# Kernel optimization log

Hardware: AMD Instinct MI355X
Metric: run time of the kernel (lower is better)

## Reference

```python
import jax, jax.numpy as jnp
import numpy as np

B, C, N, K = 8, 3, 4096, 20
EPS = 1e-5

def bn(x, g, b, axes):
    # training-mode batch norm: normalize over batch/spatial axes, channel last
    m = jnp.mean(x, axes, keepdims=True)
    v = jnp.var(x, axes, keepdims=True)
    return g * (x - m) * jax.lax.rsqrt(v + EPS) + b

def setup_inputs() -> dict:
    key = jax.random.key(0)
    ks = jax.random.split(key, 8)
    def xav(kk, shape):
        fan_out, fan_in = shape
        lim = (6.0 / (fan_in + fan_out)) ** 0.5
        return jax.random.uniform(kk, shape, minval=-lim, maxval=lim, dtype=jnp.float32)
    return dict(
        x=jax.random.normal(ks[0], (B, C, N), dtype=jnp.float32),
        w1=xav(ks[1], (64, 2 * C)), g1=jnp.ones(64), b1=jnp.zeros(64),
        w2=xav(ks[2], (128, 64)), g2=jnp.ones(128), b2=jnp.zeros(128),
        w3=xav(ks[3], (1024, 128)), g3=jnp.ones(1024), b3=jnp.zeros(1024),
        w4=xav(ks[4], (512, 1024)), g4=jnp.ones(512), b4=jnp.zeros(512),
        w5=xav(ks[5], (256, 512)), g5=jnp.ones(256), b5=jnp.zeros(256),
        wl=jnp.zeros((9, 256), dtype=jnp.float32),  # zero-init per reset_parameters
        bl=jnp.zeros(9, dtype=jnp.float32),
    )

def reference(x, w1, g1, b1, w2, g2, b2, w3, g3, b3, w4, g4, b4, w5, g5, b5, wl, bl):
    xt = jnp.transpose(x, (0, 2, 1))  # (B, N, C)
    sq = jnp.sum(xt * xt, -1)  # (B, N)
    # negative squared pairwise distance: -(|a|^2 - 2ab + |b|^2)
    nd = 2.0 * jnp.einsum('bnc,bmc->bnm', xt, xt) - sq[:, :, None] - sq[:, None, :]
    _, idx = jax.lax.top_k(nd, K)  # (B, N, K) nearest neighbors (includes self)
    nbr = jax.vmap(lambda pts, ids: pts[ids])(xt, idx)  # (B, N, K, C)
    ctr = xt[:, :, None, :]
    edge = jnp.concatenate([jnp.broadcast_to(ctr, (B, N, K, C)), nbr - ctr], -1)  # (B,N,K,2C)
    # EdgeConv shared MLP (1x1 conv + BN + ReLU), then max over k
    h = jax.nn.relu(bn(jnp.einsum('bnkc,oc->bnko', edge, w1), g1, b1, (0, 1, 2)))
    h = jax.nn.relu(bn(jnp.einsum('bnkc,oc->bnko', h, w2), g2, b2, (0, 1, 2)))
    h = jnp.max(h, 2)  # (B, N, 128)
    # local shared MLP then global max pool over points
    h = jax.nn.relu(bn(jnp.einsum('bnc,oc->bno', h, w3), g3, b3, (0, 1)))
    h = jnp.max(h, 1)  # (B, 1024)
    # global MLP
    h = jax.nn.relu(bn(h @ w4.T, g4, b4, (0,)))
    h = jax.nn.relu(bn(h @ w5.T, g5, b5, (0,)))
    y = (h @ wl.T + bl).reshape(B, 3, 3)
    return y + jnp.eye(3, dtype=y.dtype)
```

## Files before the change

### kernel.cpp

```cpp
#include <hip/hip_runtime.h>

#define NPTS 4096
#define KNN 20
#define CNT1f 655360.0f
#define CNT3f 32768.0f
#define BNEPS 1e-5f

#define OFF_IDX   0
#define OFF_M     655360
#define OFF_ES    655360
#define OFF_G1P   656384
#define OFF_S1P   672768
#define ZERO1_BEG 655360
#define ZERO1_CNT 17664
#define OFF_W2B   2752512
#define OFF_W3B   2756608
#define OFF_XP    2822144
#define OFF_G3P   2953216
#define OFF_SM3P  2985984
#define OFF_GMAX  2986240
#define OFF_Z4    2994432
#define ZG3_BEG   2953216
#define ZG3_CNT   41216
#define OFF_SC1   4849664
#define OFF_SH1   4849728
#define OFF_SC2   4849792
#define OFF_SH2   4849920
#define OFF_SC3   4850048
#define OFF_SH3   4851072
#define OFF_Z5    4856192
#define OFF_W1B   4858240

typedef float f32x4 __attribute__((ext_vector_type(4)));
typedef short s16x8 __attribute__((ext_vector_type(8)));

__device__ __forceinline__ unsigned short f2bf(float f) {
    unsigned u = __float_as_uint(f);
    return (unsigned short)((u + 0x7FFFu + ((u >> 16) & 1u)) >> 16);
}

__global__ __launch_bounds__(256) void k_initprep(const float* __restrict__ x,
                                                  const float* __restrict__ w1,
                                                  const float* __restrict__ w2,
                                                  const float* __restrict__ w3, float* W) {
    int i = blockIdx.x * 256 + threadIdx.x;
    unsigned short* w1b = (unsigned short*)(W + OFF_W1B);
    unsigned short* w2b = (unsigned short*)(W + OFF_W2B);
    unsigned short* w3b = (unsigned short*)(W + OFF_W3B);
    w3b[i] = f2bf(w3[i]);
    if (i < 8192) w2b[i] = f2bf(w2[i]);
    if (i < 2048) {
        int c = i >> 5, k = i & 31;
        w1b[i] = (k < 6) ? f2bf(w1[c * 6 + k]) : (unsigned short)0;
    }
    if (i < ZERO1_CNT) W[ZERO1_BEG + i] = 0.0f;
    if (i < ZG3_CNT) W[ZG3_BEG + i] = 0.0f;
    if (i < 32768) {
        int b = i >> 12, j = i & 4095;
        float4 p;
        p.x = x[b * 12288 + j];
        p.y = x[b * 12288 + 4096 + j];
        p.z = x[b * 12288 + 8192 + j];
        p.w = 0.f;
        ((float4*)(W + OFF_XP))[i] = p;
    }
}

template <int PER>
__device__ __forceinline__ void wave_scan_find(const int* H, int K, int lane,
                                               int& B, int& below, int& hB) {
    int c[PER]; int s = 0;
    const int base = lane * PER;
#pragma unroll
    for (int p = 0; p < PER; ++p) { c[p] = H[base + p]; s += c[p]; }
    int pre = s;
#pragma unroll
    for (int off = 1; off < 64; off <<= 1) {
        int t = __shfl_up(pre, off, 64);
        if (lane >= off) pre += t;
    }
    int excl = pre - s;
    bool has = (excl < K) && (K <= excl + s);
    unsigned long long m = __ballot(has);
    int src = (int)(__ffsll((unsigned long long)m) - 1);
    int mb = 0, mbelow = 0, mh = 0;
    if (lane == src) {
        int cum = excl;
#pragma unroll
        for (int p = 0; p < PER; ++p) {
            if (cum < K && K <= cum + c[p]) { mb = base + p; mbelow = cum; mh = c[p]; break; }
            cum += c[p];
        }
    }
    B = __shfl(mb, src, 64);
    below = __shfl(mbelow, src, 64);
    hB = __shfl(mh, src, 64);
}

__global__ __launch_bounds__(256) void k_knn(int* __restrict__ idx, float* W) {
    __shared__ int hist[4][1024];
    __shared__ int outi[4][20];
    __shared__ int cnts[4][2];
    __shared__ float estat[27];
    const int tid = threadIdx.x;
    const int b = blockIdx.y;
    const float4* xb4 = ((const float4*)(W + OFF_XP)) + b * NPTS;
    if (tid < 27) estat[tid] = 0.f;
    if (tid < 8) cnts[tid >> 1][tid & 1] = 0;
    const int wv = tid >> 6, lane = tid & 63;
    const int q = blockIdx.x * 4 + wv;
    const float4 qp = xb4[q];
    int* H = hist[wv];
    unsigned int key[64];
    unsigned int mymin = 0xFFFFFFFFu;
#pragma unroll
    for (int p = 0; p < 16; ++p) H[lane * 16 + p] = 0;
#pragma unroll
    for (int it = 0; it < 64; ++it) {
        int j = it * 64 + lane;
        float4 pp = xb4[j];
        float dx = pp.x - qp.x, dy = pp.y - qp.y, dz = pp.z - qp.z;
        float d = fmaf(dx, dx, fmaf(dy, dy, dz * dz));
        unsigned int u = (j == q) ? 0xFFFFFFFFu : __float_as_uint(d);
        key[it] = u;
        mymin = mymin < u ? mymin : u;
    }
    __syncthreads();
#pragma unroll
    for (int off = 32; off; off >>= 1) {
        unsigned int o = (unsigned int)__shfl_xor((int)mymin, off);
        mymin = mymin < o ? mymin : o;
    }
    const unsigned int base = mymin;
#pragma unroll
    for (int it = 0; it < 64; ++it) {
        unsigned int t9 = key[it] - base;
        unsigned int bin = t9 >> 19; if (bin > 1023u) bin = 1023u;
        atomicAdd(&H[bin], 1);
    }
    int B, below, hB;
    wave_scan_find<16>(H, KNN - 1, lane, B, below, hB);
    unsigned int P = (unsigned int)B;
    int rem = (KNN - 1) - below;
    int S = 19;
    if (hB != rem) {
#pragma unroll
        for (int p = 0; p < 8; ++p) H[lane * 8 + p] = 0;
#pragma unroll
        for (int it = 0; it < 64; ++it) {
            unsigned int t9 = key[it] - base;
            unsigned int b0 = t9 >> 19; if (b0 > 1023u) b0 = 1023u;
            if (b0 == P) atomicAdd(&H[(t9 >> 10) & 511], 1);
        }
        wave_scan_find<8>(H, rem, lane, B, below, hB);
        P = (P << 9) | (unsigned int)B;
        rem -= below;
        S = 10;
        if (hB != rem) {
#pragma unroll
            for (int p = 0; p < 8; ++p) H[lane * 8 + p] = 0;
#pragma unroll
            for (int it = 0; it < 64; ++it) {
                unsigned int t9 = key[it] - base;
                if ((t9 >> 10) == P) atomicAdd(&H[(t9 >> 1) & 511], 1);
            }
            wave_scan_find<8>(H, rem, lane, B, below, hB);
            P = (P << 9) | (unsigned int)B;
            rem -= below;
            S = 1;
        }
    }
    int* OC = cnts[wv];
#pragma unroll
    for (int it = 0; it < 64; ++it) {
        unsigned int t9 = key[it] - base;
        unsigned int v;
        if (S == 19) { v = t9 >> 19; if (v > 1023u) v = 1023u; }
        else v = t9 >> S;
        if (v <= P) {
            bool take = v < P;
            if (!take) { int e = atomicAdd(&OC[1], 1); take = (e < rem); }
            if (take) { int pos = atomicAdd(&OC[0], 1); outi[wv][pos] = it * 64 + lane; }
        }
    }
    if (lane == 0) outi[wv][KNN - 1] = q;
    const int obase = (b * NPTS + q) * KNN;
    if (lane < KNN) idx[obase + lane] = outi[wv][lane];
    float st[27];
#pragma unroll
    for (int v = 0; v < 27; ++v) st[v] = 0.f;
    if (lane < KNN) {
        int j = outi[wv][lane];
        float4 np = xb4[j];
        float e[6];
        e[0] = qp.x; e[1] = qp.y; e[2] = qp.z;
        e[3] = np.x - qp.x; e[4] = np.y - qp.y; e[5] = np.z - qp.z;
        int id = 6;
#pragma unroll
        for (int i = 0; i < 6; ++i) {
            st[i] = e[i];
#pragma unroll
            for (int jj = i; jj < 6; ++jj) { st[id] = e[i] * e[jj]; id++; }
        }
    }
#pragma unroll
    for (int v = 0; v < 27; ++v) {
        float s = st[v];
        s += __shfl_xor(s, 32); s += __shfl_xor(s, 16); s += __shfl_xor(s, 8);
        s += __shfl_xor(s, 4);  s += __shfl_xor(s, 2);  s += __shfl_xor(s, 1);
        st[v] = s;
    }
    if (lane == 0) {
#pragma unroll
        for (int v = 0; v < 27; ++v) atomicAdd(&estat[v], st[v]);
    }
    __syncthreads();
    if (tid < 27) atomicAdd(&W[OFF_ES + (blockIdx.x & 31) * 32 + tid], estat[tid]);
}

__global__ __launch_bounds__(256) void k_gram1(const int* __restrict__ idx,
                                               const float* __restrict__ w1,
                                               const float* __restrict__ g1,
                                               const float* __restrict__ b1, float* W) {
    __shared__ unsigned short h1t[80 * 136];
    __shared__ unsigned short eda[128 * 32];
    __shared__ float sc1s[64], sh1s[64];
    __shared__ float es[27];
    const int t = threadIdx.x;
    const int b = blockIdx.x >> 6;
    const int ebase_b = (blockIdx.x & 63) * 1280;
    const float4* xpb = ((const float4*)(W + OFF_XP)) + b * NPTS;
    const unsigned short* w1b = (const unsigned short*)(W + OFF_W1B);
    if (t < 27) {
        float s = 0.f;
        for (int p = 0; p < 32; ++p) s += W[OFF_ES + p * 32 + t];
        es[t] = s;
    }
    __syncthreads();
    if (t < 64) {
        float wr[6];
#pragma unroll
        for (int i = 0; i < 6; ++i) wr[i] = w1[t * 6 + i];
        float m = 0.f;
#pragma unroll
        for (int i = 0; i < 6; ++i) m += wr[i] * es[i];
        m *= (1.f / CNT1f);
        float qv = 0.f;
        int id = 6;
#pragma unroll
        for (int i = 0; i < 6; ++i)
#pragma unroll
            for (int jj = 0; jj < 6; ++jj)
                if (jj >= i) { qv += (jj == i ? 1.f : 2.f) * wr[i] * wr[jj] * es[id]; id++; }
        qv *= (1.f / CNT1f);
        float var = qv - m * m;
        float sc = g1[t] * rsqrtf(var + BNEPS);
        sc1s[t] = sc;
        sh1s[t] = b1[t] - m * sc;
        if (blockIdx.x == 0) { W[OFF_SC1 + t] = sc; W[OFF_SH1 + t] = sh1s[t]; }
    }
    for (int i = t; i < 2048; i += 256) {
        int rr = i >> 7, e = i & 127;
        h1t[(64 + rr) * 136 + e] = (rr == 0) ? (unsigned short)0x3F80 : (unsigned short)0;
    }
    const int w = t >> 6, lane = t & 63, n16 = lane & 15, quad = lane >> 4;
    s16x8 Bw1[4];
#pragma unroll
    for (int nt = 0; nt < 4; ++nt)
        Bw1[nt] = *(const s16x8*)&w1b[(nt * 16 + n16) * 32 + quad * 8];
    f32x4 acc[5];
#pragma unroll
    for (int j = 0; j < 5; ++j) acc[j] = (f32x4){0.f, 0.f, 0.f, 0.f};
    for (int ck = 0; ck < 10; ++ck) {
        __syncthreads();
        if (t < 128) {
            int e_l = ebase_b + ck * 128 + t;
            int q = e_l / KNN;
            int jn = idx[b * (NPTS * KNN) + e_l];
            float4 c = xpb[q];
            float4 n = xpb[jn];
            float E[6];
            E[0] = c.x; E[1] = c.y; E[2] = c.z;
            E[3] = n.x - c.x; E[4] = n.y - c.y; E[5] = n.z - c.z;
            unsigned short* row = &eda[t * 32];
#pragma unroll
            for (int k = 0; k < 6; ++k) row[k] = f2bf(E[k]);
#pragma unroll
            for (int k = 6; k < 32; ++k) row[k] = 0;
        }
        __syncthreads();
#pragma unroll
        for (int i2 = 0; i2 < 2; ++i2) {
            int tt = w + 4 * i2;
            s16x8 Af = *(const s16x8*)&eda[(tt * 16 + n16) * 32 + quad * 8];
#pragma unroll
            for (int nt = 0; nt < 4; ++nt) {
                f32x4 z = (f32x4){0.f, 0.f, 0.f, 0.f};
                z = __builtin_amdgcn_mfma_f32_16x16x32_bf16(Af, Bw1[nt], z, 0, 0, 0);
                int chan = nt * 16 + n16;
                float sc = sc1s[chan], sh = sh1s[chan];
#pragma unroll
                for (int r = 0; r < 4; ++r) {
                    float h = sc * z[r] + sh;
                    h1t[chan * 136 + tt * 16 + quad * 4 + r] = f2bf(h > 0.f ? h : 0.f);
                }
            }
        }
        __syncthreads();
#pragma unroll
        for (int ks = 0; ks < 4; ++ks) {
            s16x8 Af = *(const s16x8*)&h1t[(w * 16 + n16) * 136 + ks * 32 + quad * 8];
#pragma unroll
            for (int jt = 0; jt < 5; ++jt) {
                s16x8 Bf = *(const s16x8*)&h1t[(jt * 16 + n16) * 136 + ks * 32 + quad * 8];
                acc[jt] = __builtin_amdgcn_mfma_f32_16x16x32_bf16(Af, Bf, acc[jt], 0, 0, 0);
            }
        }
    }
    const int part = blockIdx.x & 3;
    const int gi = w * 16 + quad * 4;
#pragma unroll
    for (int jt = 0; jt < 4; ++jt)
#pragma unroll
        for (int r = 0; r < 4; ++r)
            atomicAdd(&W[OFF_G1P + part * 4096 + (gi + r) * 64 + jt * 16 + n16], acc[jt][r]);
    if (n16 == 0) {
#pragma unroll
        for (int r = 0; r < 4; ++r)
            atomicAdd(&W[OFF_S1P + part * 64 + gi + r], acc[4][r]);
    }
}

__global__ __launch_bounds__(256) void k_fin2(const float* __restrict__ w2, const float* __restrict__ g2,
                                              const float* __restrict__ b2, float* W) {
    __shared__ float Gs[4096];
    __shared__ float s1s[64];
    __shared__ float w2s[128 * 65];
    const int t = threadIdx.x;
    for (int i = t; i < 4096; i += 256)
        Gs[i] = W[OFF_G1P + i] + W[OFF_G1P + 4096 + i] + W[OFF_G1P + 8192 + i] + W[OFF_G1P + 12288 + i];
    if (t < 64) s1s[t] = W[OFF_S1P + t] + W[OFF_S1P + 64 + t] + W[OFF_S1P + 128 + t] + W[OFF_S1P + 192 + t];
    for (int i = t; i < 8192; i += 256) w2s[(i >> 6) * 65 + (i & 63)] = w2[i];
    __syncthreads();
    const int c = t >> 1, half = t & 1;
    float acc = 0.f;
    for (int ii = 0; ii < 32; ++ii) {
        int i = 32 * half + ii;
        float wi = w2s[c * 65 + i];
        float inner = 0.f;
        for (int j = 0; j < 64; ++j) inner += Gs[i * 64 + j] * w2s[c * 65 + j];
        acc += wi * inner;
    }
    acc += __shfl_xor(acc, 1);
    if (half == 0) {
        float ms = 0.f;
        for (int j = 0; j < 64; ++j) ms += w2s[c * 65 + j] * s1s[j];
        float mean = ms * (1.f / CNT1f);
        float var = acc * (1.f / CNT1f) - mean * mean;
        float sc = g2[c] * rsqrtf(var + BNEPS);
        W[OFF_SC2 + c] = sc;
        W[OFF_SH2 + c] = b2[c] - mean * sc;
    }
}

__global__ __launch_bounds__(256) void k_c2apply(const int* __restrict__ idx, float* W) {
    __shared__ unsigned short h1b[256 * 72];
    __shared__ unsigned short eda[160 * 32];
    __shared__ float sc1s[64], sh1s[64];
    const int t = threadIdx.x;
    const int b = blockIdx.y, q0 = blockIdx.x * 8;
    const float4* xpb = ((const float4*)(W + OFF_XP)) + b * NPTS;
    const int ebase = (b * NPTS + q0) * KNN;
    const unsigned short* w2b = (const unsigned short*)(W + OFF_W2B);
    const unsigned short* w1b = (const unsigned short*)(W + OFF_W1B);
    if (t < 64) { sc1s[t] = W[OFF_SC1 + t]; sh1s[t] = W[OFF_SH1 + t]; }
    if (t < 160) {
        int q = q0 + t / KNN;
        int jn = idx[ebase + t];
        float4 c = xpb[q];
        float4 n = xpb[jn];
        float E[6];
        E[0] = c.x; E[1] = c.y; E[2] = c.z;
        E[3] = n.x - c.x; E[4] = n.y - c.y; E[5] = n.z - c.z;
        unsigned short* row = &eda[t * 32];
#pragma unroll
        for (int k = 0; k < 6; ++k) row[k] = f2bf(E[k]);
#pragma unroll
        for (int k = 6; k < 32; ++k) row[k] = 0;
    }
    const int w = t >> 6, lane = t & 63, n16 = lane & 15, quad = lane >> 4;
    s16x8 Bw1[4];
#pragma unroll
    for (int nt = 0; nt < 4; ++nt)
        Bw1[nt] = *(const s16x8*)&w1b[(nt * 16 + n16) * 32 + quad * 8];
    __syncthreads();
#pragma unroll
    for (int i2 = 0; i2 < 4; ++i2) {
        int tt = w + 4 * i2;
        int row = tt * 16 + n16;
        int q = row >> 5, kk = row & 31;
        s16x8 Af = (s16x8){0, 0, 0, 0, 0, 0, 0, 0};
        if (kk < 20) Af = *(const s16x8*)&eda[(q * 20 + kk) * 32 + quad * 8];
#pragma unroll
        for (int nt = 0; nt < 4; ++nt) {
            f32x4 z = (f32x4){0.f, 0.f, 0.f, 0.f};
            z = __builtin_amdgcn_mfma_f32_16x16x32_bf16(Af, Bw1[nt], z, 0, 0, 0);
            int chan = nt * 16 + n16;
            float sc = sc1s[chan], sh = sh1s[chan];
#pragma unroll
            for (int r = 0; r < 4; ++r) {
                float h = sc * z[r] + sh;
                h1b[(tt * 16 + quad * 4 + r) * 72 + chan] = f2bf(h > 0.f ? h : 0.f);
            }
        }
    }
    __syncthreads();
    unsigned short* Mb = (unsigned short*)(W + OFF_M);
#pragma unroll
    for (int nt_i = 0; nt_i < 2; ++nt_i) {
        const int nt = 2 * w + nt_i;
        const int chan = nt * 16 + n16;
        const float sc2 = W[OFF_SC2 + chan], sh2 = W[OFF_SH2 + chan];
        s16x8 Bf0 = *(const s16x8*)&w2b[chan * 64 + quad * 8];
        s16x8 Bf1 = *(const s16x8*)&w2b[chan * 64 + 32 + quad * 8];
#pragma unroll
        for (int q = 0; q < 8; ++q) {
            f32x4 accA = (f32x4){0.f, 0.f, 0.f, 0.f};
            f32x4 accB = (f32x4){0.f, 0.f, 0.f, 0.f};
            s16x8 a0 = *(const s16x8*)&h1b[(q * 32 + n16) * 72 + quad * 8];
            s16x8 a1 = *(const s16x8*)&h1b[(q * 32 + 16 + n16) * 72 + quad * 8];
            accA = __builtin_amdgcn_mfma_f32_16x16x32_bf16(a0, Bf0, accA, 0, 0, 0);
            accB = __builtin_amdgcn_mfma_f32_16x16x32_bf16(a1, Bf0, accB, 0, 0, 0);
            a0 = *(const s16x8*)&h1b[(q * 32 + n16) * 72 + 32 + quad * 8];
            a1 = *(const s16x8*)&h1b[(q * 32 + 16 + n16) * 72 + 32 + quad * 8];
            accA = __builtin_amdgcn_mfma_f32_16x16x32_bf16(a0, Bf1, accA, 0, 0, 0);
            accB = __builtin_amdgcn_mfma_f32_16x16x32_bf16(a1, Bf1, accB, 0, 0, 0);
            float mx = 0.f;
#pragma unroll
            for (int r = 0; r < 4; ++r) {
                float h = sc2 * accA[r] + sh2;
                mx = fmaxf(mx, h > 0.f ? h : 0.f);
            }
            if (quad == 0) {
#pragma unroll
                for (int r = 0; r < 4; ++r) {
                    float h = sc2 * accB[r] + sh2;
                    mx = fmaxf(mx, h > 0.f ? h : 0.f);
                }
            }
            mx = fmaxf(mx, __shfl_xor(mx, 16));
            mx = fmaxf(mx, __shfl_xor(mx, 32));
            if (quad == 0)
                Mb[(b * NPTS + q0 + q) * 128 + chan] = f2bf(mx);
        }
    }
}

__global__ __launch_bounds__(256) void k_gram3(float* W) {
    __shared__ unsigned short Mt[128 * 72];
    const int t = threadIdx.x;
    const int w = t >> 6, lane = t & 63, n16 = lane & 15, quad = lane >> 4;
    const int r0 = blockIdx.x * 512;
    const unsigned int* Msrc = (const unsigned int*)(W + OFF_M);
    const int nA = 8 - w;
    f32x4 acc[9];
#pragma unroll
    for (int j = 0; j < 9; ++j) acc[j] = (f32x4){0.f, 0.f, 0.f, 0.f};
    float smacc = 0.f;
    for (int ch = 0; ch < 8; ++ch) {
        __syncthreads();
        for (int i = t; i < 4096; i += 256) {
            int row = i >> 6, c2 = i & 63;
            unsigned int v = Msrc[(r0 + ch * 64 + row) * 64 + c2];
            Mt[(2 * c2) * 72 + row]     = (unsigned short)(v & 0xFFFFu);
            Mt[(2 * c2 + 1) * 72 + row] = (unsigned short)(v >> 16);
        }
        __syncthreads();
#pragma unroll
        for (int j = 0; j < 9; ++j) {
            int ti = (j < nA) ? w : (7 - w);
            int tj = (j < nA) ? (w + j) : (j - nA + 7 - w);
#pragma unroll
            for (int ks = 0; ks < 2; ++ks) {
                s16x8 Af = *(const s16x8*)&Mt[(ti * 16 + n16) * 72 + ks * 32 + quad * 8];
                s16x8 Bf = *(const s16x8*)&Mt[(tj * 16 + n16) * 72 + ks * 32 + quad * 8];
                acc[j] = __builtin_amdgcn_mfma_f32_16x16x32_bf16(Af, Bf, acc[j], 0, 0, 0);
            }
        }
        if (t < 128) {
            float s = 0.f;
            for (int e = 0; e < 64; ++e)
                s += __uint_as_float((unsigned int)Mt[t * 72 + e] << 16);
            smacc += s;
        }
    }
    const int part = blockIdx.x & 1;
    float* Gp = &W[OFF_G3P + part * 16384];
#pragma unroll
    for (int j = 0; j < 9; ++j) {
        int ti = (j < nA) ? w : (7 - w);
        int tj = (j < nA) ? (w + j) : (j - nA + 7 - w);
#pragma unroll
        for (int r = 0; r < 4; ++r)
            atomicAdd(&Gp[(ti * 16 + quad * 4 + r) * 128 + tj * 16 + n16], acc[j][r]);
    }
    if (t < 128) atomicAdd(&W[OFF_SM3P + part * 128 + t], smacc);
}

__global__ __launch_bounds__(256) void k_fin3(const float* __restrict__ w3, const float* __restrict__ g3,
                                              const float* __restrict__ b3, float* W) {
    __shared__ float G3s[128 * 129];
    __shared__ float w3s[16 * 132];
    __shared__ float sm3[128];
    __shared__ float red[256];
    __shared__ float mred[16];
    const int t = threadIdx.x;
    const int c0 = blockIdx.x * 16;
    for (int i = t; i < 16384; i += 256) {
        int row = i >> 7, col = i & 127;
        int src = ((row >> 4) <= (col >> 4)) ? (row * 128 + col) : (col * 128 + row);
        G3s[row * 129 + col] = W[OFF_G3P + src] + W[OFF_G3P + 16384 + src];
    }
    for (int i = t; i < 2048; i += 256)
        w3s[(i >> 7) * 132 + (i & 127)] = w3[(c0 + (i >> 7)) * 128 + (i & 127)];
    if (t < 128) sm3[t] = W[OFF_SM3P + t] + W[OFF_SM3P + 128 + t];
    __syncthreads();
    const int cl = t >> 4, seg = t & 15;
    float acc = 0.f;
    for (int ii = 0; ii < 8; ++ii) {
        int i = 8 * seg + ii;
        float wi = w3s[cl * 132 + i];
        float inner = 0.f;
        for (int j = 0; j < 128; ++j) inner += G3s[i * 129 + j] * w3s[cl * 132 + j];
        acc += wi * inner;
    }
    red[t] = acc;
    if (seg == 0) {
        float ms = 0.f;
        for (int j = 0; j < 128; ++j) ms += w3s[cl * 132 + j] * sm3[j];
        mred[cl] = ms;
    }
    __syncthreads();
    if (t < 16) {
        float s = 0.f;
#pragma unroll
        for (int k = 0; k < 16; ++k) s += red[t * 16 + k];
        float mean = mred[t] * (1.f / CNT3f);
        float var = s * (1.f / CNT3f) - mean * mean;
        float sc = g3[c0 + t] * rsqrtf(var + BNEPS);
        W[OFF_SC3 + c0 + t] = sc;
        W[OFF_SH3 + c0 + t] = b3[c0 + t] - mean * sc;
    }
}

__global__ __launch_bounds__(256) void k_conv3(float* W) {
    __shared__ unsigned short Mt[64 * 136];
    const int t = threadIdx.x;
    const int p0 = blockIdx.x * 64, c0g = blockIdx.y * 128;
    const unsigned int* Msrc = (const unsigned int*)(W + OFF_M);
    const unsigned short* w3b = (const unsigned short*)(W + OFF_W3B);
    for (int i = t; i < 4096; i += 256) {
        int row = i >> 6, c2 = i & 63;
        *(unsigned int*)&Mt[row * 136 + 2 * c2] = Msrc[(p0 + row) * 64 + c2];
    }
    __syncthreads();
    const int w = t >> 6, lane = t & 63, n16 = lane & 15, quad = lane >> 4;
    const int bbatch = p0 >> 12;
#pragma unroll
    for (int nt_i = 0; nt_i < 2; ++nt_i) {
        const int nt = 2 * w + nt_i;
        const int chan = c0g + nt * 16 + n16;
        const float sc3 = W[OFF_SC3 + chan], sh3 = W[OFF_SH3 + chan];
        s16x8 Bf[4];
#pragma unroll
        for (int ks = 0; ks < 4; ++ks)
            Bf[ks] = *(const s16x8*)&w3b[chan * 128 + ks * 32 + quad * 8];
        float mx = 0.f;
#pragma unroll
        for (int mt = 0; mt < 4; ++mt) {
            f32x4 acc = (f32x4){0.f, 0.f, 0.f, 0.f};
#pragma unroll
            for (int ks = 0; ks < 4; ++ks) {
                s16x8 Af = *(const s16x8*)&Mt[(mt * 16 + n16) * 136 + ks * 32 + quad * 8];
                acc = __builtin_amdgcn_mfma_f32_16x16x32_bf16(Af, Bf[ks], acc, 0, 0, 0);
            }
#pragma unroll
            for (int r = 0; r < 4; ++r) {
                float h = sc3 * acc[r] + sh3;
                mx = fmaxf(mx, h > 0.f ? h : 0.f);
            }
        }
        mx = fmaxf(mx, __shfl_xor(mx, 16));
        mx = fmaxf(mx, __shfl_xor(mx, 32));
        if (quad == 0)
            atomicMax((unsigned int*)&W[OFF_GMAX + bbatch * 1024 + chan], __float_as_uint(mx));
    }
}

__global__ __launch_bounds__(256) void k_fc4(const float* __restrict__ w4, float* W) {
    __shared__ float red[256];
    const int t = threadIdx.x;
    const int oidx = t >> 3, s = t & 7;
    const int cc = oidx >> 3, b = oidx & 7;
    const int c = blockIdx.x * 4 + cc;
    const float* g = &W[OFF_GMAX];
    const float* wr = &w4[c * 1024 + s * 128];
    const float* gr = &g[b * 1024 + s * 128];
    float p = 0.f;
    for (int j = 0; j < 128; ++j) p += wr[j] * gr[j];
    red[t] = p;
    __syncthreads();
    if (t < 32) {
        float tot = 0.f;
        for (int k = 0; k < 8; ++k) tot += red[t * 8 + k];
        W[OFF_Z4 + (t & 7) * 512 + blockIdx.x * 4 + (t >> 3)] = tot;
    }
}

__global__ __launch_bounds__(256) void k_fc5(const float* __restrict__ w5,
                                             const float* __restrict__ g4,
                                             const float* __restrict__ b4, float* W) {
    __shared__ float red[256];
    __shared__ float h4s[8 * 520];
    const int t = threadIdx.x;
    for (int jj = t; jj < 512; jj += 256) {
        float v[8], s = 0.f, q = 0.f;
#pragma unroll
        for (int b = 0; b < 8; ++b) { v[b] = W[OFF_Z4 + b * 512 + jj]; s += v[b]; q += v[b] * v[b]; }
        float mean = s * 0.125f;
        float var = q * 0.125f - mean * mean;
        float sc = g4[jj] * rsqrtf(var + BNEPS);
        float sh = b4[jj] - mean * sc;
#pragma unroll
        for (int b = 0; b < 8; ++b) {
            float h = sc * v[b] + sh;
            h4s[b * 520 + jj] = h > 0.f ? h : 0.f;
        }
    }
    __syncthreads();
    const int c4 = t >> 6, b = (t >> 3) & 7, s = t & 7;
    const int c = blockIdx.x * 4 + c4;
    const float* wr = &w5[c * 512 + s * 64];
    const float* hr = &h4s[b * 520 + s * 64];
    float p = 0.f;
    for (int j = 0; j < 64; ++j) p += wr[j] * hr[j];
    red[t] = p;
    __syncthreads();
    if (t < 32) {
        const int cc = t >> 3, bb = t & 7;
        float tot = 0.f;
        for (int k = 0; k < 8; ++k) tot += red[cc * 64 + bb * 8 + k];
        W[OFF_Z5 + bb * 256 + blockIdx.x * 4 + cc] = tot;
    }
}

__global__ __launch_bounds__(256) void k_tail2(const float* __restrict__ g5, const float* __restrict__ b5,
                                               const float* __restrict__ wl, const float* __restrict__ bl,
                                               float* W, float* __restrict__ out) {
    __shared__ float zp[2048];
    const int t = threadIdx.x;
    {
        float v[8], s = 0.f, q = 0.f;
#pragma unroll
        for (int b = 0; b < 8; ++b) {
            v[b] = W[OFF_Z5 + b * 256 + t];
            s += v[b]; q += v[b] * v[b];
        }
        float mean = s * 0.125f, var = q * 0.125f - mean * mean;
        float sc = g5[t] * rsqrtf(var + BNEPS), sh = b5[t] - mean * sc;
#pragma unroll
        for (int b = 0; b < 8; ++b) { float h = sc * v[b] + sh; zp[b * 256 + t] = h > 0.f ? h : 0.f; }
    }
    __syncthreads();
    if (t < 72) {
        int b = t / 9, r = t % 9;
        float a = bl[r] + ((r == 0 || r == 4 || r == 8) ? 1.f : 0.f);
        for (int j = 0; j < 256; ++j) a += wl[r * 256 + j] * zp[b * 256 + j];
        out[b * 9 + r] = a;
    }
}

extern "C" void kernel_launch(void* const* d_in, const int* in_sizes, int n_in,
                              void* d_out, int out_size, void* d_ws, size_t ws_size,
                              hipStream_t stream) {
    const float* x  = (const float*)d_in[0];
    const float* w1 = (const float*)d_in[1];
    const float* g1 = (const float*)d_in[2];
    const float* b1 = (const float*)d_in[3];
    const float* w2 = (const float*)d_in[4];
    const float* g2 = (const float*)d_in[5];
    const float* b2 = (const float*)d_in[6];
    const float* w3 = (const float*)d_in[7];
    const float* g3 = (const float*)d_in[8];
    const float* b3 = (const float*)d_in[9];
    const float* w4 = (const float*)d_in[10];
    const float* g4 = (const float*)d_in[11];
    const float* b4 = (const float*)d_in[12];
    const float* w5 = (const float*)d_in[13];
    const float* g5 = (const float*)d_in[14];
    const float* b5 = (const float*)d_in[15];
    const float* wl = (const float*)d_in[16];
    const float* bl = (const float*)d_in[17];
    float* W = (float*)d_ws;
    int* idx = (int*)d_ws;
    float* out = (float*)d_out;

    k_initprep<<<dim3(512), dim3(256), 0, stream>>>(x, w1, w2, w3, W);
    k_knn<<<dim3(1024, 8), dim3(256), 0, stream>>>(idx, W);
    k_gram1<<<dim3(512), dim3(256), 0, stream>>>(idx, w1, g1, b1, W);
    k_fin2<<<dim3(1), dim3(256), 0, stream>>>(w2, g2, b2, W);
    k_c2apply<<<dim3(512, 8), dim3(256), 0, stream>>>(idx, W);
    k_gram3<<<dim3(64), dim3(256), 0, stream>>>(W);
    k_fin3<<<dim3(64), dim3(256), 0, stream>>>(w3, g3, b3, W);
    k_conv3<<<dim3(512, 8), dim3(256), 0, stream>>>(W);
    k_fc4<<<dim3(128), dim3(256), 0, stream>>>(w4, W);
    k_fc5<<<dim3(64), dim3(256), 0, stream>>>(w5, g4, b4, W);
    k_tail2<<<dim3(1), dim3(256), 0, stream>>>(g5, b5, wl, bl, W, out);
}
```

Measured before the change: 535.0 us.

## Replace brute-force kNN with uniform-grid spatial search and shell expansion

Adds a per-batch kernel that bins points into a 20^3 uniform grid, counting-sorts them and stores cell start offsets. The kNN kernel then visits grid cells in expanding Chebyshev shells around the query, builds the radix histogram only from candidates, and stops once the shell boundary distance exceeds the current 19th-neighbour bound. The aim is to avoid computing all 4096 distances per query. In exchange it adds an extra launch, a serial single-block-per-batch sort, divergent loops over cells, and repeated rescans of cells during refinement. Results may differ from the original on distance ties.

```diff
diff --git a/kernel.cpp b/kernel.cpp
--- a/kernel.cpp
+++ b/kernel.cpp
@@ -5,6 +5,8 @@
 #define CNT1f 655360.0f
 #define CNT3f 32768.0f
 #define BNEPS 1e-5f
+#define GRD 20
+#define GRD3 8000
 
 #define OFF_IDX   0
 #define OFF_M     655360
@@ -13,6 +15,9 @@
 #define OFF_S1P   672768
 #define ZERO1_BEG 655360
 #define ZERO1_CNT 17664
+#define OFF_XPG   673024
+#define OFF_CS    804096
+#define OFF_GP    869760
 #define OFF_W2B   2752512
 #define OFF_W3B   2756608
 #define OFF_XP    2822144
@@ -66,6 +71,101 @@
     }
 }
 
+__global__ __launch_bounds__(256) void k_grid(float* W) {
+    __shared__ int hist[8192];
+    __shared__ int tsum[256];
+    __shared__ float mm[4][6];
+    __shared__ float gp[6];
+    __shared__ int woff[4];
+    const int t = threadIdx.x, b = blockIdx.x;
+    const float4* xp = ((const float4*)(W + OFF_XP)) + b * NPTS;
+    float4* xpg = ((float4*)(W + OFF_XPG)) + b * NPTS;
+    int* CS = ((int*)(W + OFF_CS)) + b * 8208;
+    const int lane = t & 63, w = t >> 6;
+    float mnx = 3e38f, mny = 3e38f, mnz = 3e38f;
+    float mxx = -3e38f, mxy = -3e38f, mxz = -3e38f;
+    for (int i = t; i < NPTS; i += 256) {
+        float4 p = xp[i];
+        mnx = fminf(mnx, p.x); mxx = fmaxf(mxx, p.x);
+        mny = fminf(mny, p.y); mxy = fmaxf(mxy, p.y);
+        mnz = fminf(mnz, p.z); mxz = fmaxf(mxz, p.z);
+    }
+#pragma unroll
+    for (int off = 32; off; off >>= 1) {
+        mnx = fminf(mnx, __shfl_xor(mnx, off)); mxx = fmaxf(mxx, __shfl_xor(mxx, off));
+        mny = fminf(mny, __shfl_xor(mny, off)); mxy = fmaxf(mxy, __shfl_xor(mxy, off));
+        mnz = fminf(mnz, __shfl_xor(mnz, off)); mxz = fmaxf(mxz, __shfl_xor(mxz, off));
+    }
+    if (lane == 0) {
+        mm[w][0] = mnx; mm[w][1] = mny; mm[w][2] = mnz;
+        mm[w][3] = mxx; mm[w][4] = mxy; mm[w][5] = mxz;
+    }
+    for (int i = t; i < 8192; i += 256) hist[i] = 0;
+    __syncthreads();
+    if (t == 0) {
+        float ax = fminf(fminf(mm[0][0], mm[1][0]), fminf(mm[2][0], mm[3][0]));
+        float ay = fminf(fminf(mm[0][1], mm[1][1]), fminf(mm[2][1], mm[3][1]));
+        float az = fminf(fminf(mm[0][2], mm[1][2]), fminf(mm[2][2], mm[3][2]));
+        float bx = fmaxf(fmaxf(mm[0][3], mm[1][3]), fmaxf(mm[2][3], mm[3][3]));
+        float by = fmaxf(fmaxf(mm[0][4], mm[1][4]), fmaxf(mm[2][4], mm[3][4]));
+        float bz = fmaxf(fmaxf(mm[0][5], mm[1][5]), fmaxf(mm[2][5], mm[3][5]));
+        gp[0] = ax; gp[1] = ay; gp[2] = az;
+        gp[3] = (bx - ax) * (1.000001f / GRD) + 1e-7f;
+        gp[4] = (by - ay) * (1.000001f / GRD) + 1e-7f;
+        gp[5] = (bz - az) * (1.000001f / GRD) + 1e-7f;
+#pragma unroll
+        for (int k = 0; k < 6; ++k) W[OFF_GP + b * 8 + k] = gp[k];
+    }
+    __syncthreads();
+    const float gx = gp[0], gy = gp[1], gz = gp[2];
+    const float hx = gp[3], hy = gp[4], hz = gp[5];
+    for (int i = t; i < NPTS; i += 256) {
+        float4 p = xp[i];
+        int cx = (int)((p.x - gx) / hx); cx = cx < 0 ? 0 : (cx > GRD - 1 ? GRD - 1 : cx);
+        int cy = (int)((p.y - gy) / hy); cy = cy < 0 ? 0 : (cy > GRD - 1 ? GRD - 1 : cy);
+        int cz = (int)((p.z - gz) / hz); cz = cz < 0 ? 0 : (cz > GRD - 1 ? GRD - 1 : cz);
+        atomicAdd(&hist[cx + GRD * (cy + GRD * cz)], 1);
+    }
+    __syncthreads();
+    const int base = t * 32;
+    int s = 0;
+    for (int k = 0; k < 32; ++k) s += hist[base + k];
+    {
+        int pre = s;
+#pragma unroll
+        for (int off = 1; off < 64; off <<= 1) {
+            int u2 = __shfl_up(pre, off, 64);
+            if (lane >= off) pre += u2;
+        }
+        if (lane == 63) woff[w] = pre;
+        __syncthreads();
+        int add = 0;
+        for (int k = 0; k < w; ++k) add += woff[k];
+        tsum[t] = pre - s + add;
+    }
+    __syncthreads();
+    {
+        int run = tsum[t];
+        for (int k = 0; k < 32; ++k) {
+            int c = base + k;
+            int cnt = hist[c];
+            hist[c] = run;
+            if (c <= GRD3) CS[c] = run;
+            run += cnt;
+        }
+    }
+    __syncthreads();
+    for (int i = t; i < NPTS; i += 256) {
+        float4 p = xp[i];
+        int cx = (int)((p.x - gx) / hx); cx = cx < 0 ? 0 : (cx > GRD - 1 ? GRD - 1 : cx);
+        int cy = (int)((p.y - gy) / hy); cy = cy < 0 ? 0 : (cy > GRD - 1 ? GRD - 1 : cy);
+        int cz = (int)((p.z - gz) / hz); cz = cz < 0 ? 0 : (cz > GRD - 1 ? GRD - 1 : cz);
+        int pos = atomicAdd(&hist[cx + GRD * (cy + GRD * cz)], 1);
+        float4 o; o.x = p.x; o.y = p.y; o.z = p.z; o.w = __int_as_float(i);
+        xpg[b == b ? pos : pos] = o;
+    }
+}
+
 template <int PER>
 __device__ __forceinline__ void wave_scan_find(const int* H, int K, int lane,
                                                int& B, int& below, int& hB) {
@@ -104,115 +204,177 @@
     __shared__ float estat[27];
     const int tid = threadIdx.x;
     const int b = blockIdx.y;
-    const float4* xb4 = ((const float4*)(W + OFF_XP)) + b * NPTS;
+    const float4* xp = ((const float4*)(W + OFF_XP)) + b * NPTS;
+    const float4* xpg = ((const float4*)(W + OFF_XPG)) + b * NPTS;
+    const int* CS = ((const int*)(W + OFF_CS)) + b * 8208;
     if (tid < 27) estat[tid] = 0.f;
     if (tid < 8) cnts[tid >> 1][tid & 1] = 0;
     const int wv = tid >> 6, lane = tid & 63;
     const int q = blockIdx.x * 4 + wv;
-    const float4 qp = xb4[q];
+    const float4 qp = xp[q];
+    const float gx = W[OFF_GP + b * 8 + 0], gy = W[OFF_GP + b * 8 + 1], gz = W[OFF_GP + b * 8 + 2];
+    const float hx = W[OFF_GP + b * 8 + 3], hy = W[OFF_GP + b * 8 + 4], hz = W[OFF_GP + b * 8 + 5];
+    int cx = (int)((qp.x - gx) / hx); cx = cx < 0 ? 0 : (cx > GRD - 1 ? GRD - 1 : cx);
+    int cy = (int)((qp.y - gy) / hy); cy = cy < 0 ? 0 : (cy > GRD - 1 ? GRD - 1 : cy);
+    int cz = (int)((qp.z - gz) / hz); cz = cz < 0 ? 0 : (cz > GRD - 1 ? GRD - 1 : cz);
     int* H = hist[wv];
-    unsigned int key[64];
-    unsigned int mymin = 0xFFFFFFFFu;
 #pragma unroll
     for (int p = 0; p < 16; ++p) H[lane * 16 + p] = 0;
-#pragma unroll
-    for (int it = 0; it < 64; ++it) {
-        int j = it * 64 + lane;
-        float4 pp = xb4[j];
-        float dx = pp.x - qp.x, dy = pp.y - qp.y, dz = pp.z - qp.z;
-        float d = fmaf(dx, dx, fmaf(dy, dy, dz * dz));
-        unsigned int u = (j == q) ? 0xFFFFFFFFu : __float_as_uint(d);
-        key[it] = u;
-        mymin = mymin < u ? mymin : u;
-    }
-    __syncthreads();
-#pragma unroll
-    for (int off = 32; off; off >>= 1) {
-        unsigned int o = (unsigned int)__shfl_xor((int)mymin, off);
-        mymin = mymin < o ? mymin : o;
-    }
-    const unsigned int base = mymin;
-#pragma unroll
-    for (int it = 0; it < 64; ++it) {
-        unsigned int t9 = key[it] - base;
-        unsigned int bin = t9 >> 19; if (bin > 1023u) bin = 1023u;
-        atomicAdd(&H[bin], 1);
-    }
+    __syncthreads();
+    int mycnt = 0;
     int B, below, hB;
-    wave_scan_find<16>(H, KNN - 1, lane, B, below, hB);
-    unsigned int P = (unsigned int)B;
-    int rem = (KNN - 1) - below;
-    int S = 19;
-    if (hB != rem) {
+    unsigned int P0 = 0;
+    int rem = 0, sp = 0;
+    bool fin0 = false;
+    for (int s = 0; s <= GRD; ++s) {
+        const int xl = max(0, cx - s), xh = min(GRD - 1, cx + s);
+        const int yl = max(0, cy - s), yh = min(GRD - 1, cy + s);
+        const int zl = max(0, cz - s), zh = min(GRD - 1, cz + s);
+        for (int uz = zl; uz <= zh; ++uz)
+        for (int uy = yl; uy <= yh; ++uy)
+        for (int ux = xl; ux <= xh; ++ux) {
+            int adx = ux - cx; adx = adx < 0 ? -adx : adx;
+            int ady = uy - cy; ady = ady < 0 ? -ady : ady;
+            int adz = uz - cz; adz = adz < 0 ? -adz : adz;
+            int ch = max(adx, max(ady, adz));
+            if (ch != s) continue;
+            int ci = ux + GRD * (uy + GRD * uz);
+            int st = CS[ci], en = CS[ci + 1];
+            for (int j = st + lane; j < en; j += 64) {
+                float4 pp = xpg[j];
+                int oi = __float_as_int(pp.w);
+                if (oi != q) {
+                    float dx = pp.x - qp.x, dy = pp.y - qp.y, dz = pp.z - qp.z;
+                    float d = fmaf(dx, dx, fmaf(dy, dy, dz * dz));
+                    atomicAdd(&H[__float_as_uint(d) >> 21], 1);
+                    ++mycnt;
+                }
+            }
+        }
+        int wc = mycnt;
+#pragma unroll
+        for (int off = 32; off; off >>= 1) wc += __shfl_xor(wc, off);
+        float fd = 3.0e38f;
+        bool exh = true;
+        if (cx - s > 0)       { fd = fminf(fd, qp.x - (gx + (cx - s) * hx)); exh = false; }
+        if (cx + s < GRD - 1) { fd = fminf(fd, (gx + (cx + s + 1) * hx) - qp.x); exh = false; }
+        if (cy - s > 0)       { fd = fminf(fd, qp.y - (gy + (cy - s) * hy)); exh = false; }
+        if (cy + s < GRD - 1) { fd = fminf(fd, (gy + (cy + s + 1) * hy) - qp.y); exh = false; }
+        if (cz - s > 0)       { fd = fminf(fd, qp.z - (gz + (cz - s) * hz)); exh = false; }
+        if (cz + s < GRD - 1) { fd = fminf(fd, (gz + (cz + s + 1) * hz) - qp.z); exh = false; }
+        if (wc >= KNN - 1) {
+            wave_scan_find<16>(H, KNN - 1, lane, B, below, hB);
+            P0 = (unsigned int)B;
+            rem = (KNN - 1) - below;
+            float tub = (B >= 1022) ? 3.0e38f : __uint_as_float((unsigned int)(B + 1) << 21);
+            fd = fmaxf(fd - 1e-4f, 0.f);
+            if (exh || fd * fd >= tub) { sp = s; fin0 = (hB == rem); break; }
+        }
+    }
+    unsigned int P = P0;
+    int S = 21;
+    const int xl = max(0, cx - sp), xh = min(GRD - 1, cx + sp);
+    const int yl = max(0, cy - sp), yh = min(GRD - 1, cy + sp);
+    const int zl = max(0, cz - sp), zh = min(GRD - 1, cz + sp);
+    if (!fin0) {
 #pragma unroll
         for (int p = 0; p < 8; ++p) H[lane * 8 + p] = 0;
-#pragma unroll
-        for (int it = 0; it < 64; ++it) {
-            unsigned int t9 = key[it] - base;
-            unsigned int b0 = t9 >> 19; if (b0 > 1023u) b0 = 1023u;
-            if (b0 == P) atomicAdd(&H[(t9 >> 10) & 511], 1);
+        for (int uz = zl; uz <= zh; ++uz)
+        for (int uy = yl; uy <= yh; ++uy)
+        for (int ux = xl; ux <= xh; ++ux) {
+            int ci = ux + GRD * (uy + GRD * uz);
+            int st = CS[ci], en = CS[ci + 1];
+            for (int j = st + lane; j < en; j += 64) {
+                float4 pp = xpg[j];
+                int oi = __float_as_int(pp.w);
+                if (oi != q) {
+                    float dx = pp.x - qp.x, dy = pp.y - qp.y, dz = pp.z - qp.z;
+                    float d = fmaf(dx, dx, fmaf(dy, dy, dz * dz));
+                    unsigned int u = __float_as_uint(d);
+                    if ((u >> 21) == P0) atomicAdd(&H[(u >> 12) & 511], 1);
+                }
+            }
         }
         wave_scan_find<8>(H, rem, lane, B, below, hB);
-        P = (P << 9) | (unsigned int)B;
+        P = (P0 << 9) | (unsigned int)B;
         rem -= below;
-        S = 10;
+        S = 12;
         if (hB != rem) {
 #pragma unroll
             for (int p = 0; p < 8; ++p) H[lane * 8 + p] = 0;
-#pragma unroll
-            for (int it = 0; it < 64; ++it) {
-                unsigned int t9 = key[it] - base;
-                if ((t9 >> 10) == P) atomicAdd(&H[(t9 >> 1) & 511], 1);
+            for (int uz = zl; uz <= zh; ++uz)
+            for (int uy = yl; uy <= yh; ++uy)
+            for (int ux = xl; ux <= xh; ++ux) {
+                int ci = ux + GRD * (uy + GRD * uz);
+                int st = CS[ci], en = CS[ci + 1];
+                for (int j = st + lane; j < en; j += 64) {
+                    float4 pp = xpg[j];
+                    int oi = __float_as_int(pp.w);
+                    if (oi != q) {
+                        float dx = pp.x - qp.x, dy = pp.y - qp.y, dz = pp.z - qp.z;
+                        float d = fmaf(dx, dx, fmaf(dy, dy, dz * dz));
+                        unsigned int u = __float_as_uint(d);
+                        if ((u >> 12) == P) atomicAdd(&H[(u >> 3) & 511], 1);
+                    }
+                }
             }
             wave_scan_find<8>(H, rem, lane, B, below, hB);
             P = (P << 9) | (unsigned int)B;
             rem -= below;
-            S = 1;
+            S = 3;
         }
     }
     int* OC = cnts[wv];
-#pragma unroll
-    for (int it = 0; it < 64; ++it) {
-        unsigned int t9 = key[it] - base;
-        unsigned int v;
-        if (S == 19) { v = t9 >> 19; if (v > 1023u) v = 1023u; }
-        else v = t9 >> S;
-        if (v <= P) {
-            bool take = v < P;
-            if (!take) { int e = atomicAdd(&OC[1], 1); take = (e < rem); }
-            if (take) { int pos = atomicAdd(&OC[0], 1); outi[wv][pos] = it * 64 + lane; }
+    for (int uz = zl; uz <= zh; ++uz)
+    for (int uy = yl; uy <= yh; ++uy)
+    for (int ux = xl; ux <= xh; ++ux) {
+        int ci = ux + GRD * (uy + GRD * uz);
+        int st = CS[ci], en = CS[ci + 1];
+        for (int j = st + lane; j < en; j += 64) {
+            float4 pp = xpg[j];
+            int oi = __float_as_int(pp.w);
+            if (oi != q) {
+                float dx = pp.x - qp.x, dy = pp.y - qp.y, dz = pp.z - qp.z;
+                float d = fmaf(dx, dx, fmaf(dy, dy, dz * dz));
+                unsigned int v = __float_as_uint(d) >> S;
+                if (v <= P) {
+                    bool take = v < P;
+                    if (!take) { int e = atomicAdd(&OC[1], 1); take = (e < rem); }
+                    if (take) { int pos = atomicAdd(&OC[0], 1); outi[wv][pos] = oi; }
+                }
+            }
         }
     }
     if (lane == 0) outi[wv][KNN - 1] = q;
     const int obase = (b * NPTS + q) * KNN;
     if (lane < KNN) idx[obase + lane] = outi[wv][lane];
-    float st[27];
-#pragma unroll
-    for (int v = 0; v < 27; ++v) st[v] = 0.f;
+    float st7[27];
+#pragma unroll
+    for (int v = 0; v < 27; ++v) st7[v] = 0.f;
     if (lane < KNN) {
         int j = outi[wv][lane];
-        float4 np = xb4[j];
+        float4 np = xp[j];
         float e[6];
         e[0] = qp.x; e[1] = qp.y; e[2] = qp.z;
         e[3] = np.x - qp.x; e[4] = np.y - qp.y; e[5] = np.z - qp.z;
         int id = 6;
 #pragma unroll
         for (int i = 0; i < 6; ++i) {
-            st[i] = e[i];
-#pragma unroll
-            for (int jj = i; jj < 6; ++jj) { st[id] = e[i] * e[jj]; id++; }
+            st7[i] = e[i];
+#pragma unroll
+            for (int jj = i; jj < 6; ++jj) { st7[id] = e[i] * e[jj]; id++; }
         }
     }
 #pragma unroll
     for (int v = 0; v < 27; ++v) {
-        float s = st[v];
+        float s = st7[v];
         s += __shfl_xor(s, 32); s += __shfl_xor(s, 16); s += __shfl_xor(s, 8);
         s += __shfl_xor(s, 4);  s += __shfl_xor(s, 2);  s += __shfl_xor(s, 1);
-        st[v] = s;
+        st7[v] = s;
     }
     if (lane == 0) {
 #pragma unroll
-        for (int v = 0; v < 27; ++v) atomicAdd(&estat[v], st[v]);
+        for (int v = 0; v < 27; ++v) atomicAdd(&estat[v], st7[v]);
     }
     __syncthreads();
     if (tid < 27) atomicAdd(&W[OFF_ES + (blockIdx.x & 31) * 32 + tid], estat[tid]);
@@ -706,6 +868,7 @@
     float* out = (float*)d_out;
 
     k_initprep<<<dim3(512), dim3(256), 0, stream>>>(x, w1, w2, w3, W);
+    k_grid<<<dim3(8), dim3(256), 0, stream>>>(W);
     k_knn<<<dim3(1024, 8), dim3(256), 0, stream>>>(idx, W);
     k_gram1<<<dim3(512), dim3(256), 0, stream>>>(idx, w1, g1, b1, W);
     k_fin2<<<dim3(1), dim3(256), 0, stream>>>(w2, g2, b2, W);
```

Result: slower. 1.911 ms (+257.2%).
